# Kernel tuning notes

Hardware: AMD Instinct MI355X
Metric: run time of the kernel (lower is better)

## Reference

```python
import jax, jax.numpy as jnp
import numpy as np

QMIN, QMAX = 0.0, 255.0  # uint8 export range

def _round_half_away(x):
    # torch _round_nearest_without_round: round half away from zero
    return jnp.where(x < 0, -jnp.floor(-x + 0.5), jnp.floor(x + 0.5))

def setup_inputs() -> dict:
    key = jax.random.key(0)
    k = jax.random.split(key, 7)
    B, S, DIN, DOUT = 2, 2048, 2048, 8192
    x = jax.random.normal(k[0], (B, S, DIN), dtype=jnp.float32)
    # per-tensor activation qparams (keep scale away from 0)
    a_scale = jax.random.uniform(k[1], (1,), dtype=jnp.float32) * 0.05 + 0.01
    a_zp = jax.random.randint(k[2], (1,), 100, 156, dtype=jnp.int32)
    # pre-quantized uint8 weight stored as int32, per-out-channel qparams
    weight_q = jax.random.randint(k[3], (DOUT, DIN), 0, 256, dtype=jnp.int32)
    w_scale = jax.random.uniform(k[4], (DOUT,), dtype=jnp.float32) * 0.02 + 0.001
    w_zp = jax.random.randint(k[5], (DOUT,), 100, 156, dtype=jnp.int32)
    bias = jax.random.normal(k[6], (DOUT,), dtype=jnp.float32)
    return {"x": x, "a_scale": a_scale, "a_zp": a_zp, "weight_q": weight_q,
            "w_scale": w_scale, "w_zp": w_zp, "bias": bias}

def reference(x, a_scale, a_zp, weight_q, w_scale, w_zp, bias):
    dt = x.dtype
    # --- activation fake-quant (ExportAffineQuantizer, per-tensor) ---
    s = a_scale.astype(dt).reshape((1,) * x.ndim)
    z = a_zp.astype(dt).reshape((1,) * x.ndim)
    x_q = jnp.clip(_round_half_away(x / s) + z, QMIN, QMAX)
    x_dq = (x_q - z) * s
    # --- weight dequant (ExportWeightBackedLinear, ch_axis=0) ---
    # W: [out, in] = (w_q - zp) * scale, broadcast over in-dim
    W = (weight_q.astype(dt) - w_zp.astype(dt)[:, None]) * w_scale.astype(dt)[:, None]
    # --- linear: [B,S,in] @ [in,out] + bias ---
    return jnp.einsum('bsk,ok->bso', x_dq, W) + bias.astype(dt)
```

## Files before the change

kernel.cpp:

```cpp
#include <hip/hip_runtime.h>
#include <hip/hip_bf16.h>

#define M_DIM 4096
#define K_DIM 2048
#define N_DIM 8192

#define BM 128
#define BN 128
#define BK 64

typedef int   int32x4 __attribute__((ext_vector_type(4)));
typedef float f32x4   __attribute__((ext_vector_type(4)));

#define XC_OFF 0
#define WC_OFF 8388608UL
#define RX_OFF 25165824UL
#define AL_OFF 25182208UL
#define G_OFF  25214976UL
#define F0_OFF 25247744UL

__device__ __forceinline__ int pack4(int a, int b, int c, int d) {
    return (a & 255) | ((b & 255) << 8) | ((c & 255) << 16) | ((d & 255) << 24);
}

__global__ __launch_bounds__(256) void prep_x_kernel(
    const float4* __restrict__ x, signed char* __restrict__ xc, int* __restrict__ rx,
    const float* __restrict__ a_scale, const int* __restrict__ a_zp)
{
    const int row = blockIdx.x;
    const int tid = threadIdx.x;
    const float s = a_scale[0];
    const float z = (float)a_zp[0];
    int sum = 0;
    int* xci = (int*)(xc + (size_t)row * K_DIM);
    const float4* xr = x + (size_t)row * (K_DIM / 4);
    #pragma unroll
    for (int it = 0; it < 2; ++it) {
        int qi = tid + it * 256;
        float4 v = xr[qi];
        int q0 = (int)(fminf(fmaxf(roundf(v.x / s) + z, 0.f), 255.f)) - 128;
        int q1 = (int)(fminf(fmaxf(roundf(v.y / s) + z, 0.f), 255.f)) - 128;
        int q2 = (int)(fminf(fmaxf(roundf(v.z / s) + z, 0.f), 255.f)) - 128;
        int q3 = (int)(fminf(fmaxf(roundf(v.w / s) + z, 0.f), 255.f)) - 128;
        sum += q0 + q1 + q2 + q3;
        xci[qi] = pack4(q0, q1, q2, q3);
    }
    #pragma unroll
    for (int off = 32; off > 0; off >>= 1) sum += __shfl_down(sum, off);
    __shared__ int wsum[4];
    if ((tid & 63) == 0) wsum[tid >> 6] = sum;
    __syncthreads();
    if (tid == 0) rx[row] = wsum[0] + wsum[1] + wsum[2] + wsum[3];
}

__global__ __launch_bounds__(256) void prep_w_kernel(
    const int4* __restrict__ wq, signed char* __restrict__ wc,
    int* __restrict__ al, float* __restrict__ g, float* __restrict__ F0,
    const float* __restrict__ a_scale, const int* __restrict__ a_zp,
    const float* __restrict__ w_scale, const int* __restrict__ w_zp,
    const float* __restrict__ bias)
{
    const int o   = blockIdx.x;
    const int tid = threadIdx.x;
    int sum = 0;
    int* wci = (int*)(wc + (size_t)o * K_DIM);
    const int4* wr = wq + (size_t)o * (K_DIM / 4);
    #pragma unroll
    for (int it = 0; it < 2; ++it) {
        int qi = tid + it * 256;
        int4 v = wr[qi];
        int q0 = v.x - 128, q1 = v.y - 128, q2 = v.z - 128, q3 = v.w - 128;
        sum += q0 + q1 + q2 + q3;
        wci[qi] = pack4(q0, q1, q2, q3);
    }
    #pragma unroll
    for (int off = 32; off > 0; off >>= 1) sum += __shfl_down(sum, off);
    __shared__ int wsum[4];
    if ((tid & 63) == 0) wsum[tid >> 6] = sum;
    __syncthreads();
    if (tid == 0) {
        int rw    = wsum[0] + wsum[1] + wsum[2] + wsum[3];
        int alpha = 128 - w_zp[o];
        int beta  = 128 - a_zp[0];
        int C0    = beta * (rw + K_DIM * alpha);
        float gg  = a_scale[0] * w_scale[o];
        al[o] = alpha;
        g[o]  = gg;
        F0[o] = gg * (float)C0 + bias[o];
    }
}


__device__ __forceinline__ void glds16(const void* gptr, void* lptr) {
    __builtin_amdgcn_global_load_lds(
        (const __attribute__((address_space(1))) void*)gptr,
        (__attribute__((address_space(3))) void*)lptr,
        16, 0, 0);
}

__global__ __launch_bounds__(256) void gemm_i8_kernel(
    const signed char* __restrict__ A,
    const signed char* __restrict__ Bw,
    const int*   __restrict__ rx,
    const int*   __restrict__ al,
    const float* __restrict__ g,
    const float* __restrict__ F0,
    float* __restrict__ C)
{
    __shared__ __align__(16) signed char As[BM * BK];
    __shared__ __align__(16) signed char Bs[BN * BK];

    const int tid  = threadIdx.x;
    const int lane = tid & 63;
    const int wave = tid >> 6;
    const int wr   = wave >> 1;
    const int wc   = wave & 1;

    const int bn0 = blockIdx.x * BN;
    const int bm0 = blockIdx.y * BM;

    int32x4 acc[4][4];
    #pragma unroll
    for (int i = 0; i < 4; ++i)
        #pragma unroll
        for (int j = 0; j < 4; ++j)
            acc[i][j] = (int32x4){0, 0, 0, 0};

    const int c0 = tid, c1 = tid + 256;
    const int r0 = c0 >> 2, cb0 = (c0 & 3) * 16;
    const int r1 = c1 >> 2, cb1 = (c1 & 3) * 16;

    const signed char* Abase = A  + (size_t)bm0 * K_DIM;
    const signed char* Bbase = Bw + (size_t)bn0 * K_DIM;

    const int fr = lane & 15;
    const int kg = (lane >> 4) * 16;

    for (int k0 = 0; k0 < K_DIM; k0 += BK) {
        __syncthreads();
        glds16(Abase + (size_t)r0 * K_DIM + k0 + cb0, &As[c0 * 16]);
        glds16(Abase + (size_t)r1 * K_DIM + k0 + cb1, &As[c1 * 16]);
        glds16(Bbase + (size_t)r0 * K_DIM + k0 + cb0, &Bs[c0 * 16]);
        glds16(Bbase + (size_t)r1 * K_DIM + k0 + cb1, &Bs[c1 * 16]);
        __syncthreads();

        int32x4 af[4], bf[4];
        #pragma unroll
        for (int i = 0; i < 4; ++i) {
            int row = wr * 64 + i * 16 + fr;
            af[i] = *reinterpret_cast<const int32x4*>(&As[row * BK + kg]);
        }
        #pragma unroll
        for (int j = 0; j < 4; ++j) {
            int row = wc * 64 + j * 16 + fr;
            bf[j] = *reinterpret_cast<const int32x4*>(&Bs[row * BK + kg]);
        }
        #pragma unroll
        for (int i = 0; i < 4; ++i)
            #pragma unroll
            for (int j = 0; j < 4; ++j)
                acc[i][j] = __builtin_amdgcn_mfma_i32_16x16x64_i8(af[i], bf[j], acc[i][j], 0, 0, 0);
    }

    const int fq = lane >> 4;
    int rxl[4][4];
    #pragma unroll
    for (int i = 0; i < 4; ++i)
        #pragma unroll
        for (int v = 0; v < 4; ++v)
            rxl[i][v] = rx[bm0 + wr * 64 + i * 16 + fq * 4 + v];

    #pragma unroll
    for (int j = 0; j < 4; ++j) {
        int col = bn0 + wc * 64 + j * 16 + fr;
        int   av = al[col];
        float gv = g[col];
        float fv = F0[col];
        #pragma unroll
        for (int i = 0; i < 4; ++i) {
            int rowg = bm0 + wr * 64 + i * 16 + fq * 4;
            #pragma unroll
            for (int v = 0; v < 4; ++v) {
                int t = acc[i][j][v] + av * rxl[i][v];
                C[(size_t)(rowg + v) * N_DIM + col] = fmaf(gv, (float)t, fv);
            }
        }
    }
}


extern "C" void kernel_launch(void* const* d_in, const int* in_sizes, int n_in,
                              void* d_out, int out_size, void* d_ws, size_t ws_size,
                              hipStream_t stream) {
    const float* x        = (const float*)d_in[0];
    const float* a_scale  = (const float*)d_in[1];
    const int*   a_zp     = (const int*)d_in[2];
    const int*   weight_q = (const int*)d_in[3];
    const float* w_scale  = (const float*)d_in[4];
    const int*   w_zp     = (const int*)d_in[5];
    const float* bias     = (const float*)d_in[6];
    float*       out      = (float*)d_out;

    char* ws = (char*)d_ws;
    signed char* xc = (signed char*)(ws + XC_OFF);
    signed char* wc = (signed char*)(ws + WC_OFF);
    int*   rx = (int*)(ws + RX_OFF);
    int*   al = (int*)(ws + AL_OFF);
    float* g  = (float*)(ws + G_OFF);
    float* F0 = (float*)(ws + F0_OFF);

    prep_x_kernel<<<M_DIM, 256, 0, stream>>>((const float4*)x, xc, rx, a_scale, a_zp);
    prep_w_kernel<<<N_DIM, 256, 0, stream>>>((const int4*)weight_q, wc, al, g, F0,
                                             a_scale, a_zp, w_scale, w_zp, bias);

    dim3 grid(N_DIM / BN, M_DIM / BM);
    gemm_i8_kernel<<<grid, 256, 0, stream>>>(xc, wc, rx, al, g, F0, out);
}
```

Before: 292.7 us.

## Rewrite int8 GEMM with 256x256 tiles, 4-stage LDS pipeline, 32x32 MFMA

Replaces the single-buffered 128x128 GEMM with a 512-thread, 256x256-tile kernel. It uses a 4-deep ring of global-to-LDS async loads with vmcnt-based waits, XOR-swizzled LDS columns to avoid bank conflicts, 32x32x32 int8 MFMA, s_setprio around the math, and a swizzled block order for L2 reuse. The goal is to hide global load latency and cut redundant tile loads. In exchange it needs 128KB of dynamic LDS, allowing only one block per CU, and carries hand-tuned barrier and wait counts that are fragile.

New measurement: 292.1 us. About the same (-0.2%).

```diff
diff --git a/kernel.cpp b/kernel.cpp
--- a/kernel.cpp
+++ b/kernel.cpp
@@ -5,12 +5,10 @@
 #define K_DIM 2048
 #define N_DIM 8192
 
-#define BM 128
-#define BN 128
-#define BK 64
-
-typedef int   int32x4 __attribute__((ext_vector_type(4)));
-typedef float f32x4   __attribute__((ext_vector_type(4)));
+#define NT 32
+
+typedef int   int32x4  __attribute__((ext_vector_type(4)));
+typedef int   int32x16 __attribute__((ext_vector_type(16)));
 
 #define XC_OFF 0
 #define WC_OFF 8388608UL
@@ -94,11 +92,10 @@
 __device__ __forceinline__ void glds16(const void* gptr, void* lptr) {
     __builtin_amdgcn_global_load_lds(
         (const __attribute__((address_space(1))) void*)gptr,
-        (__attribute__((address_space(3))) void*)lptr,
-        16, 0, 0);
-}
-
-__global__ __launch_bounds__(256) void gemm_i8_kernel(
+        (__attribute__((address_space(3))) void*)lptr, 16, 0, 0);
+}
+
+__global__ __launch_bounds__(512) void gemm_i8_kernel(
     const signed char* __restrict__ A,
     const signed char* __restrict__ Bw,
     const int*   __restrict__ rx,
@@ -107,85 +104,116 @@
     const float* __restrict__ F0,
     float* __restrict__ C)
 {
-    __shared__ __align__(16) signed char As[BM * BK];
-    __shared__ __align__(16) signed char Bs[BN * BK];
+    extern __shared__ signed char lds[];
+    signed char* ldsA = lds;
+    signed char* ldsB = lds + 65536;
 
     const int tid  = threadIdx.x;
     const int lane = tid & 63;
     const int wave = tid >> 6;
-    const int wr   = wave >> 1;
-    const int wc   = wave & 1;
-
-    const int bn0 = blockIdx.x * BN;
-    const int bm0 = blockIdx.y * BM;
-
-    int32x4 acc[4][4];
-    #pragma unroll
-    for (int i = 0; i < 4; ++i)
+    const int wr   = wave >> 2;
+    const int wc   = wave & 3;
+    const int l31  = lane & 31;
+    const int lk   = lane >> 5;
+    const int rsw  = (l31 >> 1) & 3;
+
+    const int bid = blockIdx.x;
+    const int swz = (bid & 7) * 64 + (bid >> 3);
+    const int bn0 = (swz & 31) * 256;
+    const int bm0 = (swz >> 5) * 256;
+
+    const int  sr  = tid >> 2;
+    const int  spc = (tid & 3) ^ ((sr >> 1) & 3);
+    const signed char* srcA0 = A  + (size_t)(bm0 + sr) * K_DIM + spc * 16;
+    const signed char* srcA1 = srcA0 + (size_t)128 * K_DIM;
+    const signed char* srcB0 = Bw + (size_t)(bn0 + sr) * K_DIM + spc * 16;
+    const signed char* srcB1 = srcB0 + (size_t)128 * K_DIM;
+    signed char* dstA0 = ldsA + tid * 16;
+    signed char* dstB0 = ldsB + tid * 16;
+
+#define STAGE_A(s) { const int kof = (s) * 64; const int bo = ((s) & 3) * 16384; \
+    glds16(srcA0 + kof, dstA0 + bo); glds16(srcA1 + kof, dstA0 + bo + 8192); }
+#define STAGE_B(s) { const int kof = (s) * 64; const int bo = ((s) & 3) * 16384; \
+    glds16(srcB0 + kof, dstB0 + bo); glds16(srcB1 + kof, dstB0 + bo + 8192); }
+
+    int arowb[4], browb[2];
+    #pragma unroll
+    for (int im = 0; im < 4; ++im) arowb[im] = (wr * 128 + im * 32 + l31) * 64;
+    #pragma unroll
+    for (int jn = 0; jn < 2; ++jn) browb[jn] = (wc * 64 + jn * 32 + l31) * 64;
+    const int aoff0 = ((0 + lk) ^ rsw) << 4;
+    const int aoff1 = ((2 + lk) ^ rsw) << 4;
+
+    int32x16 acc[4][2];
+    #pragma unroll
+    for (int im = 0; im < 4; ++im)
         #pragma unroll
-        for (int j = 0; j < 4; ++j)
-            acc[i][j] = (int32x4){0, 0, 0, 0};
-
-    const int c0 = tid, c1 = tid + 256;
-    const int r0 = c0 >> 2, cb0 = (c0 & 3) * 16;
-    const int r1 = c1 >> 2, cb1 = (c1 & 3) * 16;
-
-    const signed char* Abase = A  + (size_t)bm0 * K_DIM;
-    const signed char* Bbase = Bw + (size_t)bn0 * K_DIM;
-
-    const int fr = lane & 15;
-    const int kg = (lane >> 4) * 16;
-
-    for (int k0 = 0; k0 < K_DIM; k0 += BK) {
-        __syncthreads();
-        glds16(Abase + (size_t)r0 * K_DIM + k0 + cb0, &As[c0 * 16]);
-        glds16(Abase + (size_t)r1 * K_DIM + k0 + cb1, &As[c1 * 16]);
-        glds16(Bbase + (size_t)r0 * K_DIM + k0 + cb0, &Bs[c0 * 16]);
-        glds16(Bbase + (size_t)r1 * K_DIM + k0 + cb1, &Bs[c1 * 16]);
-        __syncthreads();
-
-        int32x4 af[4], bf[4];
+        for (int jn = 0; jn < 2; ++jn)
+            acc[im][jn] = (int32x16)(0);
+
+#define TILE_PH(T, AOFF, STAGE_STMT) { \
+    const int bo_ = ((T) & 3) * 16384; \
+    int32x4 af[4], bf[2]; \
+    _Pragma("unroll") for (int im = 0; im < 4; ++im) \
+        af[im] = *(const int32x4*)(ldsA + bo_ + arowb[im] + (AOFF)); \
+    _Pragma("unroll") for (int jn = 0; jn < 2; ++jn) \
+        bf[jn] = *(const int32x4*)(ldsB + bo_ + browb[jn] + (AOFF)); \
+    STAGE_STMT; \
+    __builtin_amdgcn_s_barrier(); \
+    __builtin_amdgcn_s_setprio(1); \
+    _Pragma("unroll") for (int im = 0; im < 4; ++im) \
+        _Pragma("unroll") for (int jn = 0; jn < 2; ++jn) \
+            acc[im][jn] = __builtin_amdgcn_mfma_i32_32x32x32_i8(af[im], bf[jn], acc[im][jn], 0, 0, 0); \
+    __builtin_amdgcn_s_setprio(0); \
+}
+
+#define MIDBAR __builtin_amdgcn_s_barrier();
+#define BOUND(N) { asm volatile("s_waitcnt vmcnt(" #N ")" ::: "memory"); __builtin_amdgcn_s_barrier(); }
+
+    STAGE_A(0); STAGE_B(0);
+    STAGE_A(1); STAGE_B(1);
+    STAGE_A(2); STAGE_B(2);
+    asm volatile("s_waitcnt vmcnt(8)" ::: "memory");
+    __builtin_amdgcn_s_barrier();
+
+    #pragma unroll 1
+    for (int t = 0; t < 29; ++t) {
+        TILE_PH(t, aoff0, STAGE_A(t + 3)); MIDBAR;
+        TILE_PH(t, aoff1, STAGE_B(t + 3));
+        BOUND(8);
+    }
+    TILE_PH(29, aoff0, ((void)0)); MIDBAR;
+    TILE_PH(29, aoff1, ((void)0)); BOUND(4);
+    TILE_PH(30, aoff0, ((void)0)); MIDBAR;
+    TILE_PH(30, aoff1, ((void)0)); BOUND(0);
+    TILE_PH(31, aoff0, ((void)0)); MIDBAR;
+    TILE_PH(31, aoff1, ((void)0));
+
+    #pragma unroll
+    for (int im = 0; im < 4; ++im) {
+        int rxv[16];
         #pragma unroll
-        for (int i = 0; i < 4; ++i) {
-            int row = wr * 64 + i * 16 + fr;
-            af[i] = *reinterpret_cast<const int32x4*>(&As[row * BK + kg]);
-        }
+        for (int r = 0; r < 16; ++r)
+            rxv[r] = rx[bm0 + wr * 128 + im * 32 + (r & 3) + 8 * (r >> 2) + 4 * lk];
         #pragma unroll
-        for (int j = 0; j < 4; ++j) {
-            int row = wc * 64 + j * 16 + fr;
-            bf[j] = *reinterpret_cast<const int32x4*>(&Bs[row * BK + kg]);
-        }
-        #pragma unroll
-        for (int i = 0; i < 4; ++i)
+        for (int jn = 0; jn < 2; ++jn) {
+            const int col = bn0 + wc * 64 + jn * 32 + l31;
+            const float gg = g[col];
+            const float ff = F0[col];
+            const int   aa = al[col];
             #pragma unroll
-            for (int j = 0; j < 4; ++j)
-                acc[i][j] = __builtin_amdgcn_mfma_i32_16x16x64_i8(af[i], bf[j], acc[i][j], 0, 0, 0);
-    }
-
-    const int fq = lane >> 4;
-    int rxl[4][4];
-    #pragma unroll
-    for (int i = 0; i < 4; ++i)
-        #pragma unroll
-        for (int v = 0; v < 4; ++v)
-            rxl[i][v] = rx[bm0 + wr * 64 + i * 16 + fq * 4 + v];
-
-    #pragma unroll
-    for (int j = 0; j < 4; ++j) {
-        int col = bn0 + wc * 64 + j * 16 + fr;
-        int   av = al[col];
-        float gv = g[col];
-        float fv = F0[col];
-        #pragma unroll
-        for (int i = 0; i < 4; ++i) {
-            int rowg = bm0 + wr * 64 + i * 16 + fq * 4;
-            #pragma unroll
-            for (int v = 0; v < 4; ++v) {
-                int t = acc[i][j][v] + av * rxl[i][v];
-                C[(size_t)(rowg + v) * N_DIM + col] = fmaf(gv, (float)t, fv);
+            for (int r = 0; r < 16; ++r) {
+                const int grow = bm0 + wr * 128 + im * 32 + (r & 3) + 8 * (r >> 2) + 4 * lk;
+                const int tv = acc[im][jn][r] + aa * rxv[r];
+                C[(size_t)grow * N_DIM + col] = fmaf(gg, (float)tv, ff);
             }
         }
     }
+#undef TILE_PH
+#undef STAGE_A
+#undef STAGE_B
+#undef MIDBAR
+#undef BOUND
 }
 
 
@@ -213,6 +241,5 @@
     prep_w_kernel<<<N_DIM, 256, 0, stream>>>((const int4*)weight_q, wc, al, g, F0,
                                              a_scale, a_zp, w_scale, w_zp, bias);
 
-    dim3 grid(N_DIM / BN, M_DIM / BM);
-    gemm_i8_kernel<<<grid, 256, 0, stream>>>(xc, wc, rx, al, g, F0, out);
-}
+    gemm_i8_kernel<<<512, 512, 131072, stream>>>(xc, wc, rx, al, g, F0, out);
+}
```
